# Optimization experiments

Measured on AMD Instinct MI355X. Metric: run time of the kernel, lower is better.

## Reference

```python
import jax, jax.numpy as jnp
import numpy as np

HEADS = 16
NEG_INF = -1e30


def rel_shift(t):
    # t: [b, h, i, j] with i == j; Transformer-XL style relative shift
    b, h, i, j = t.shape
    t = jnp.pad(t, ((0, 0), (0, 0), (0, 0), (1, 0)))  # zero pad on last dim front
    t = t.reshape(b, h, j + 1, i)[:, :, 1:]
    return t.reshape(b, h, i, j)


def setup_inputs() -> dict:
    key = jax.random.key(0)
    ks = jax.random.split(key, 8)
    b, n, dim = 2, 2048, 1024
    d_head = dim // HEADS
    w = 0.02
    return {
        "x": jax.random.normal(ks[0], (b, n, dim), dtype=jnp.float32),
        "pos_emb": jax.random.normal(ks[1], (n, dim), dtype=jnp.float32),
        "Wq": jax.random.normal(ks[2], (dim, dim), dtype=jnp.float32) * w,
        "bq": jnp.zeros((dim,), dtype=jnp.float32),
        "Wkv": jax.random.normal(ks[3], (dim, 2 * dim), dtype=jnp.float32) * w,
        "bkv": jnp.zeros((2 * dim,), dtype=jnp.float32),
        "Wp": jax.random.normal(ks[4], (dim, d_head), dtype=jnp.float32) * w,
        "bp": jnp.zeros((d_head,), dtype=jnp.float32),
        "Wo": jax.random.normal(ks[5], (dim, dim), dtype=jnp.float32) * w,
        "bo": jnp.zeros((dim,), dtype=jnp.float32),
    }


def reference(x, pos_emb, Wq, bq, Wkv, bkv, Wp, bp, Wo, bo):
    b, n, dim = x.shape
    h = HEADS
    d = dim // h
    scale = d ** -0.5

    q = (x @ Wq + bq).reshape(b, n, h, d).transpose(0, 2, 1, 3)  # b h n d
    kv = x @ Wkv + bkv
    k, v = jnp.split(kv, 2, axis=-1)
    k = k.reshape(b, n, h, d).transpose(0, 2, 1, 3)
    v = v.reshape(b, n, h, d).transpose(0, 2, 1, 3)

    dots = jnp.einsum('bhid,bhjd->bhij', q, k) * scale

    # relative position bias
    p = pos_emb @ Wp + bp  # [n, d]
    pos_attn = jnp.einsum('bhid,jd->bhij', q, p) * scale
    dots = dots + rel_shift(pos_attn)

    # causal mask
    causal = jnp.triu(jnp.ones((n, n), dtype=bool), 1)
    dots = jnp.where(causal[None, None], NEG_INF, dots)

    attn = jax.nn.softmax(dots, axis=-1)
    out = jnp.einsum('bhij,bhjd->bhid', attn, v)
    out = out.transpose(0, 2, 1, 3).reshape(b, n, dim)
    return out @ Wo + bo
```

## Files before the change

### kernel.cpp

```cpp
#include <hip/hip_runtime.h>
#include <hip/hip_bf16.h>
#include <cstdint>
#include <cstddef>

#define SEQ_N 2048
#define DIM   1024
#define NHEAD 16
#define DH    64

typedef __bf16 bf16;
typedef __attribute__((ext_vector_type(8))) __bf16 bf16x8;
typedef __attribute__((ext_vector_type(4))) __bf16 bf16x4;
typedef __attribute__((ext_vector_type(4))) float f32x4;

__device__ __forceinline__ void gl_lds16(const bf16* g, bf16* l) {
    __builtin_amdgcn_global_load_lds(
        (const __attribute__((address_space(1))) unsigned int*)g,
        (__attribute__((address_space(3))) unsigned int*)l, 16, 0, 0);
}

__global__ __launch_bounds__(256) void prep_kernel(
    const float* __restrict__ x, const float* __restrict__ pos,
    const float* __restrict__ Wq, const float* __restrict__ Wkv,
    const float* __restrict__ Wo, const float* __restrict__ Wp,
    bf16* __restrict__ xb, bf16* __restrict__ posb,
    bf16* __restrict__ WqkvT, bf16* __restrict__ WoT, bf16* __restrict__ WpT)
{
    int bid = blockIdx.x;
    if (bid < 6144) {
        const int NX = 4096 * 1024;
        int i = (bid * 256 + threadIdx.x) * 4;
        if (i < NX) {
            float4 v = *(const float4*)&x[i];
            xb[i + 0] = (bf16)v.x; xb[i + 1] = (bf16)v.y;
            xb[i + 2] = (bf16)v.z; xb[i + 3] = (bf16)v.w;
        } else {
            int j = i - NX;
            float4 v = *(const float4*)&pos[j];
            posb[j + 0] = (bf16)v.x; posb[j + 1] = (bf16)v.y;
            posb[j + 2] = (bf16)v.z; posb[j + 3] = (bf16)v.w;
        }
        return;
    }
    __shared__ float t[32][33];
    bid -= 6144;
    const float* src; bf16* dst; int tidx, nx, N;
    if (bid < 1024)      { src = Wq;  dst = WqkvT;                       tidx = bid;        nx = 32; N = 1024; }
    else if (bid < 3072) { src = Wkv; dst = WqkvT + (size_t)1024 * 1024; tidx = bid - 1024; nx = 64; N = 2048; }
    else if (bid < 4096) { src = Wo;  dst = WoT;                         tidx = bid - 3072; nx = 32; N = 1024; }
    else                 { src = Wp;  dst = WpT;                         tidx = bid - 4096; nx = 2;  N = 64;   }
    int n0 = (tidx % nx) * 32, k0 = (tidx / nx) * 32;
    int tx = threadIdx.x & 31, ty = threadIdx.x >> 5;
    #pragma unroll
    for (int r = ty; r < 32; r += 8)
        t[r][tx] = src[(size_t)(k0 + r) * N + n0 + tx];
    __syncthreads();
    #pragma unroll
    for (int r = ty; r < 32; r += 8)
        dst[(size_t)(n0 + r) * 1024 + k0 + tx] = (bf16)t[tx][r];
}

__global__ __launch_bounds__(256) void qkvp_kernel(
    const bf16* __restrict__ xb, const bf16* __restrict__ WqkvT,
    const bf16* __restrict__ posb, const bf16* __restrict__ WpT,
    const float* __restrict__ bq, const float* __restrict__ bkv,
    const float* __restrict__ bp,
    bf16* __restrict__ qbuf, bf16* __restrict__ kbuf,
    bf16* __restrict__ vtbuf, bf16* __restrict__ pfrag)
{
    __shared__ __align__(16) bf16 sm[128 * 132];
    bf16* At = sm;
    bf16* Bt = sm + 128 * 64;
    const int tid = threadIdx.x, w = tid >> 6, lane = tid & 63;
    const int q = lane >> 4, ln15 = lane & 15;
    const int lr = lane >> 3, c_log = (lane & 7) ^ lr;
    const int bx = blockIdx.x, by = blockIdx.y;
    const int m0 = by * 128;

    if (bx == 24) {
        if (by >= 16) return;
        f32x4 acc[2][4] = {};
        for (int k0 = 0; k0 < 1024; k0 += 64) {
            __syncthreads();
            #pragma unroll
            for (int t = 0; t < 4; ++t)
                gl_lds16(&posb[(size_t)(m0 + 32 * w + 8 * t + lr) * 1024 + k0 + c_log * 8],
                         &At[(32 * w + 8 * t) * 64]);
            #pragma unroll
            for (int t = 0; t < 2; ++t)
                gl_lds16(&WpT[(size_t)(16 * w + 8 * t + lr) * 1024 + k0 + c_log * 8],
                         &Bt[(16 * w + 8 * t) * 64]);
            __syncthreads();
            bf16x8 bfr[2][4];
            #pragma unroll
            for (int ks = 0; ks < 2; ++ks)
                #pragma unroll
                for (int sn = 0; sn < 4; ++sn) {
                    int rb = 16 * sn + ln15;
                    bfr[ks][sn] = *(const bf16x8*)&Bt[(rb * 8 + ((4 * ks + q) ^ (rb & 7))) * 8];
                }
            #pragma unroll
            for (int sm2 = 0; sm2 < 2; ++sm2) {
                int ra = 32 * w + 16 * sm2 + ln15;
                #pragma unroll
                for (int ks = 0; ks < 2; ++ks) {
                    bf16x8 af = *(const bf16x8*)&At[(ra * 8 + ((4 * ks + q) ^ (ra & 7))) * 8];
                    #pragma unroll
                    for (int sn = 0; sn < 4; ++sn)
                        acc[sm2][sn] = __builtin_amdgcn_mfma_f32_16x16x32_bf16(
                            af, bfr[ks][sn], acc[sm2][sn], 0, 0, 0);
                }
            }
        }
        #pragma unroll
        for (int sm2 = 0; sm2 < 2; ++sm2)
            #pragma unroll
            for (int sn = 0; sn < 4; ++sn)
                #pragma unroll
                for (int r = 0; r < 4; ++r) {
                    int row = m0 + 32 * w + 16 * sm2 + 4 * q + r;
                    int d = 16 * sn + ln15;
                    int sb = row >> 4, lnp = row & 15;
                    int ks2 = d >> 5, qd = (d >> 3) & 3, e = d & 7;
                    pfrag[(((size_t)sb * 2 + ks2) * 64 + qd * 16 + lnp) * 8 + e] =
                        (bf16)(acc[sm2][sn][r] + bp[d]);
                }
        return;
    }

    const int n0 = bx * 128;
    const int wm = w >> 1, wn = w & 1;
    f32x4 acc[4][4] = {};

    for (int k0 = 0; k0 < 1024; k0 += 64) {
        __syncthreads();
        #pragma unroll
        for (int t = 0; t < 4; ++t) {
            int r = 32 * w + 8 * t + lr;
            gl_lds16(&xb[(size_t)(m0 + r) * 1024 + k0 + c_log * 8],
                     &At[(32 * w + 8 * t) * 64]);
            gl_lds16(&WqkvT[(size_t)(n0 + r) * 1024 + k0 + c_log * 8],
                     &Bt[(32 * w + 8 * t) * 64]);
        }
        __syncthreads();

        bf16x8 af[2][4], bfr[2][4];
        #pragma unroll
        for (int ks = 0; ks < 2; ++ks)
            #pragma unroll
            for (int s = 0; s < 4; ++s) {
                int ra = 64 * wm + 16 * s + ln15;
                af[ks][s]  = *(const bf16x8*)&At[(ra * 8 + ((4 * ks + q) ^ (ra & 7))) * 8];
                int rb = 64 * wn + 16 * s + ln15;
                bfr[ks][s] = *(const bf16x8*)&Bt[(rb * 8 + ((4 * ks + q) ^ (rb & 7))) * 8];
            }
        #pragma unroll
        for (int ks = 0; ks < 2; ++ks)
            #pragma unroll
            for (int si = 0; si < 4; ++si)
                #pragma unroll
                for (int sj = 0; sj < 4; ++sj)
                    acc[si][sj] = __builtin_amdgcn_mfma_f32_16x16x32_bf16(
                        af[ks][si], bfr[ks][sj], acc[si][sj], 0, 0, 0);
    }

    if (bx < 16) {
        #pragma unroll
        for (int si = 0; si < 4; ++si)
            #pragma unroll
            for (int sj = 0; sj < 4; ++sj)
                #pragma unroll
                for (int r = 0; r < 4; ++r) {
                    int row = m0 + 64 * wm + 16 * si + 4 * q + r;
                    int col = n0 + 64 * wn + 16 * sj + ln15;
                    float v = acc[si][sj][r] + (col < 1024 ? bq[col] : bkv[col - 1024]);
                    if (col < 1024) qbuf[(size_t)row * 1024 + col] = (bf16)v;
                    else            kbuf[(size_t)row * 1024 + (col - 1024)] = (bf16)v;
                }
    } else {
        __syncthreads();
        #pragma unroll
        for (int si = 0; si < 4; ++si)
            #pragma unroll
            for (int sj = 0; sj < 4; ++sj) {
                int dL = 64 * wn + 16 * sj + ln15;
                int tL = 64 * wm + 16 * si + 4 * q;
                float bias = bkv[1024 + (bx - 16) * 128 + dL];
                bf16x4 o4;
                #pragma unroll
                for (int r = 0; r < 4; ++r)
                    o4[r] = (bf16)(acc[si][sj][r] + bias);
                *(bf16x4*)&sm[dL * 132 + tL] = o4;
            }
        __syncthreads();
        const int b = m0 >> 11;
        const int t0 = m0 & 2047;
        const int h0 = (bx - 16) * 2;
        #pragma unroll
        for (int p = 0; p < 16; ++p) {
            int d = (tid >> 5) + 8 * p;
            int t = (tid & 31) * 4;
            bf16x4 v4 = *(const bf16x4*)&sm[d * 132 + t];
            int rowv = (b * NHEAD + h0 + (d >> 6)) * DH + (d & 63);
            *(bf16x4*)&vtbuf[(size_t)rowv * SEQ_N + t0 + t] = v4;
        }
    }
}

__global__ __launch_bounds__(256, 4) void attn_mfma_kernel(
    const bf16* __restrict__ qb,
    const bf16* __restrict__ kb,
    const bf16* __restrict__ vt,
    const bf16* __restrict__ pfrag,
    bf16* __restrict__ ob)
{
    const int bh = blockIdx.y, bi = bh >> 4, hh = bh & 15;
    const int qblk = ((blockIdx.y >> 3) & 1) ? (31 - (int)blockIdx.x)
                                             : (int)blockIdx.x;
    const int i0 = qblk << 6;
    const int tid = threadIdx.x, w = tid >> 6, lane = tid & 63;
    const int q = lane >> 4, ln15 = lane & 15;
    const int lr = lane >> 3, c_log = (lane & 7) ^ lr;

    __shared__ __align__(16) bf16 smem[17664];
    bf16* Qs  = smem;
    bf16* S2L = smem + w * 1344;
    bf16* Ks  = smem + 5376;
    bf16* Vs  = smem + 9472;
    bf16* Pw  = smem + 13568 + w * 1024;

    const bf16* qbase = qb + ((size_t)(bi * SEQ_N + i0)) * DIM + hh * DH;
    const bf16* kbase = kb + ((size_t)bi * SEQ_N) * DIM + hh * DH;
    const bf16* vbase = vt + ((size_t)(bi * NHEAD + hh) * DH) * SEQ_N;

    #pragma unroll
    for (int t = 0; t < 2; ++t)
        gl_lds16(qbase + (size_t)(16 * w + 8 * t + lr) * DIM + c_log * 8,
                 &Qs[(16 * w + 8 * t) * 64]);
    __syncthreads();
    bf16x8 qf0, qf1;
    {
        int rq = 16 * w + ln15;
        qf0 = *(const bf16x8*)&Qs[(rq * 8 + ((q    ) ^ (rq & 7))) * 8];
        qf1 = *(const bf16x8*)&Qs[(rq * 8 + ((4 + q) ^ (rq & 7))) * 8];
    }
    __syncthreads();

    const int A0 = 127 - 4 * qblk - w;
    f32x4 s2r4;
    {
        bf16x8 f0 = *(const bf16x8*)&pfrag[(((size_t)A0 * 2 + 0) * 64 + lane) * 8];
        bf16x8 f1 = *(const bf16x8*)&pfrag[(((size_t)A0 * 2 + 1) * 64 + lane) * 8];
        f32x4 a = {0.f, 0.f, 0.f, 0.f};
        a = __builtin_amdgcn_mfma_f32_16x16x32_bf16(f0, qf0, a, 0, 0, 0);
        a = __builtin_amdgcn_mfma_f32_16x16x32_bf16(f1, qf1, a, 0, 0, 0);
        s2r4 = a;
    }

    float m_run = -1e30f, l_run = 0.f;
    f32x4 O_T[4] = {};

    for (int jt = 0; jt <= qblk; ++jt) {
        const int j0 = jt << 6;

        bf16x8 pfA[4][2];
        #pragma unroll
        for (int s = 1; s <= 4; ++s) {
            int sb = A0 + 4 * jt + s;
            if (sb > 127) sb = 127;
            pfA[s-1][0] = *(const bf16x8*)&pfrag[(((size_t)sb * 2 + 0) * 64 + lane) * 8];
            pfA[s-1][1] = *(const bf16x8*)&pfrag[(((size_t)sb * 2 + 1) * 64 + lane) * 8];
        }
        #pragma unroll
        for (int t = 0; t < 2; ++t) {
            int r = 16 * w + 8 * t + lr;
            gl_lds16(kbase + (size_t)(j0 + r) * DIM + c_log * 8,
                     &Ks[(16 * w + 8 * t) * 64]);
            gl_lds16(vbase + (size_t)r * SEQ_N + j0 + c_log * 8,
                     &Vs[(16 * w + 8 * t) * 64]);
        }

        f32x4 s2r[5];
        s2r[0] = s2r4;
        #pragma unroll
        for (int s = 1; s <= 4; ++s) {
            f32x4 a = {0.f, 0.f, 0.f, 0.f};
            a = __builtin_amdgcn_mfma_f32_16x16x32_bf16(pfA[s-1][0], qf0, a, 0, 0, 0);
            a = __builtin_amdgcn_mfma_f32_16x16x32_bf16(pfA[s-1][1], qf1, a, 0, 0, 0);
            s2r[s] = a;
        }
        s2r4 = s2r[4];
        #pragma unroll
        for (int s = 0; s < 5; ++s)
            #pragma unroll
            for (int r = 0; r < 4; ++r)
                S2L[ln15 * 84 + 16 * s + 4 * q + r] = (bf16)s2r[s][r];

        __syncthreads();

        float sv[4][4];
        #pragma unroll
        for (int sn = 0; sn < 4; ++sn) {
            int rk = 16 * sn + ln15;
            bf16x8 k0f = *(const bf16x8*)&Ks[(rk * 8 + ((q    ) ^ (rk & 7))) * 8];
            bf16x8 k1f = *(const bf16x8*)&Ks[(rk * 8 + ((4 + q) ^ (rk & 7))) * 8];
            f32x4 a = {0.f, 0.f, 0.f, 0.f};
            a = __builtin_amdgcn_mfma_f32_16x16x32_bf16(k0f, qf0, a, 0, 0, 0);
            a = __builtin_amdgcn_mfma_f32_16x16x32_bf16(k1f, qf1, a, 0, 0, 0);
            #pragma unroll
            for (int r = 0; r < 4; ++r) {
                int jl = 16 * sn + 4 * q + r;
                float b = (float)S2L[ln15 * 84 + 15 - ln15 + jl];
                sv[sn][r] = (a[r] + b) * 0.125f;
            }
        }
        if (jt == qblk) {
            #pragma unroll
            for (int sn = 0; sn < 4; ++sn)
                #pragma unroll
                for (int r = 0; r < 4; ++r)
                    if (16 * sn + 4 * q + r > 16 * w + ln15)
                        sv[sn][r] = -1e30f;
        }

        float mx = sv[0][0];
        #pragma unroll
        for (int sn = 0; sn < 4; ++sn)
            #pragma unroll
            for (int r = 0; r < 4; ++r)
                mx = fmaxf(mx, sv[sn][r]);
        mx = fmaxf(mx, __shfl_xor(mx, 16));
        mx = fmaxf(mx, __shfl_xor(mx, 32));
        const float mn = fmaxf(m_run, mx);
        float sum = 0.f;
        #pragma unroll
        for (int sn = 0; sn < 4; ++sn)
            #pragma unroll
            for (int r = 0; r < 4; ++r) {
                float e = __expf(sv[sn][r] - mn);
                sv[sn][r] = e;
                sum += e;
            }
        sum += __shfl_xor(sum, 16);
        sum += __shfl_xor(sum, 32);
        const float alpha = __expf(m_run - mn);
        l_run = l_run * alpha + sum;
        m_run = mn;

        #pragma unroll
        for (int sn = 0; sn < 4; ++sn)
            #pragma unroll
            for (int r = 0; r < 4; ++r) {
                int chunk = (2 * sn + (q >> 1)) ^ (ln15 & 7);
                Pw[ln15 * 64 + chunk * 8 + 4 * (q & 1) + r] = (bf16)sv[sn][r];
            }
        #pragma unroll
        for (int sd = 0; sd < 4; ++sd)
            #pragma unroll
            for (int r = 0; r < 4; ++r)
                O_T[sd][r] *= alpha;

        __builtin_amdgcn_s_waitcnt(0);

        #pragma unroll
        for (int ks = 0; ks < 2; ++ks) {
            bf16x8 pT = *(const bf16x8*)&Pw[ln15 * 64 + (((4 * ks + q) ^ (ln15 & 7))) * 8];
            #pragma unroll
            for (int sd = 0; sd < 4; ++sd) {
                int rv = 16 * sd + ln15;
                bf16x8 vf = *(const bf16x8*)&Vs[(rv * 8 + ((4 * ks + q) ^ (rv & 7))) * 8];
                O_T[sd] = __builtin_amdgcn_mfma_f32_16x16x32_bf16(vf, pT, O_T[sd], 0, 0, 0);
            }
        }
        __syncthreads();
    }

    const float inv = 1.0f / l_run;
    const size_t row = (size_t)bi * SEQ_N + i0 + 16 * w + ln15;
    #pragma unroll
    for (int sd = 0; sd < 4; ++sd) {
        bf16x4 o4;
        #pragma unroll
        for (int r = 0; r < 4; ++r)
            o4[r] = (bf16)(O_T[sd][r] * inv);
        *(bf16x4*)&ob[row * DIM + hh * DH + 16 * sd + 4 * q] = o4;
    }
}

__global__ __launch_bounds__(256) void outproj_kernel(
    const bf16* __restrict__ ab, const bf16* __restrict__ WoT,
    const float* __restrict__ bo, float* __restrict__ out)
{
    __shared__ __align__(16) bf16 At[128 * 64];
    __shared__ __align__(16) bf16 Bt[64 * 64];
    const int tid = threadIdx.x, w = tid >> 6, lane = tid & 63;
    const int q = lane >> 4, ln15 = lane & 15;
    const int lr = lane >> 3, c_log = (lane & 7) ^ lr;
    const int m0 = blockIdx.y * 128, n0 = blockIdx.x * 64;

    f32x4 acc[2][4] = {};
    for (int k0 = 0; k0 < 1024; k0 += 64) {
        __syncthreads();
        #pragma unroll
        for (int t = 0; t < 4; ++t)
            gl_lds16(&ab[(size_t)(m0 + 32 * w + 8 * t + lr) * 1024 + k0 + c_log * 8],
                     &At[(32 * w + 8 * t) * 64]);
        #pragma unroll
        for (int t = 0; t < 2; ++t)
            gl_lds16(&WoT[(size_t)(n0 + 16 * w + 8 * t + lr) * 1024 + k0 + c_log * 8],
                     &Bt[(16 * w + 8 * t) * 64]);
        __syncthreads();

        bf16x8 bfr[2][4];
        #pragma unroll
        for (int ks = 0; ks < 2; ++ks)
            #pragma unroll
            for (int sn = 0; sn < 4; ++sn) {
                int rb = 16 * sn + ln15;
                bfr[ks][sn] = *(const bf16x8*)&Bt[(rb * 8 + ((4 * ks + q) ^ (rb & 7))) * 8];
            }
        #pragma unroll
        for (int sm2 = 0; sm2 < 2; ++sm2) {
            int ra = 32 * w + 16 * sm2 + ln15;
            #pragma unroll
            for (int ks = 0; ks < 2; ++ks) {
                bf16x8 af = *(const bf16x8*)&At[(ra * 8 + ((4 * ks + q) ^ (ra & 7))) * 8];
                #pragma unroll
                for (int sn = 0; sn < 4; ++sn)
                    acc[sm2][sn] = __builtin_amdgcn_mfma_f32_16x16x32_bf16(
                        af, bfr[ks][sn], acc[sm2][sn], 0, 0, 0);
            }
        }
    }
    #pragma unroll
    for (int sm2 = 0; sm2 < 2; ++sm2)
        #pragma unroll
        for (int sn = 0; sn < 4; ++sn) {
            int col = n0 + 16 * sn + ln15;
            float bias = bo[col];
            #pragma unroll
            for (int r = 0; r < 4; ++r) {
                int row = m0 + 32 * w + 16 * sm2 + 4 * q + r;
                out[(size_t)row * 1024 + col] = acc[sm2][sn][r] + bias;
            }
        }
}

extern "C" void kernel_launch(void* const* d_in, const int* in_sizes, int n_in,
                              void* d_out, int out_size, void* d_ws, size_t ws_size,
                              hipStream_t stream)
{
    const float* x    = (const float*)d_in[0];
    const float* pos  = (const float*)d_in[1];
    const float* Wq   = (const float*)d_in[2];
    const float* bq   = (const float*)d_in[3];
    const float* Wkv  = (const float*)d_in[4];
    const float* bkv  = (const float*)d_in[5];
    const float* Wp   = (const float*)d_in[6];
    const float* bp   = (const float*)d_in[7];
    const float* Wo   = (const float*)d_in[8];
    const float* bo   = (const float*)d_in[9];
    float* out = (float*)d_out;

    const int M = 2 * SEQ_N;
    char* ws = (char*)d_ws;
    bf16* xb     = (bf16*)ws;  ws += (size_t)M * DIM * 2;
    bf16* posb   = (bf16*)ws;  ws += (size_t)SEQ_N * DIM * 2;
    bf16* WqkvT  = (bf16*)ws;  ws += (size_t)3072 * 1024 * 2;
    bf16* WoT    = (bf16*)ws;  ws += (size_t)DIM * DIM * 2;
    bf16* WpT    = (bf16*)ws;  ws += (size_t)DH * DIM * 2;
    bf16* qbuf   = (bf16*)ws;  ws += (size_t)M * DIM * 2;
    bf16* kbuf   = (bf16*)ws;  ws += (size_t)M * DIM * 2;
    bf16* vtbuf  = (bf16*)ws;  ws += (size_t)M * DIM * 2;
    bf16* pfrag  = (bf16*)ws;  ws += (size_t)512 * 1024;
    bf16* abuf   = (bf16*)ws;

    dim3 blk(256);
    prep_kernel<<<dim3(10304), blk, 0, stream>>>(
        x, pos, Wq, Wkv, Wo, Wp, xb, posb, WqkvT, WoT, WpT);

    qkvp_kernel<<<dim3(25, 32), blk, 0, stream>>>(
        xb, WqkvT, posb, WpT, bq, bkv, bp, qbuf, kbuf, vtbuf, pfrag);

    attn_mfma_kernel<<<dim3(32, 32), blk, 0, stream>>>(
        qbuf, kbuf, vtbuf, pfrag, abuf);

    outproj_kernel<<<dim3(16, 32), blk, 0, stream>>>(
        abuf, WoT, bo, out);
}
```

Measured before the change: 246.0 us.

## Process 128 query rows per attention block with two row strips per wave

The attention kernel's query tile grows from 64 to 128 rows, and each wave now handles two 16-row strips. This lets every K/V tile loaded into shared memory, and the relative-position fragments, serve twice as many query rows. Causal masking is now computed per strip from position differences, and a wave skips key tiles lying entirely above its diagonal. The load-balancing swap now pairs block order by batch instead of head, and launch bounds drop to 2 blocks per CU. That raises register and shared-memory use and halves the grid to 512 blocks, which reduces occupancy and parallelism.

```diff
diff --git a/kernel.cpp b/kernel.cpp
--- a/kernel.cpp
+++ b/kernel.cpp
@@ -207,70 +207,81 @@
     }
 }
 
-__global__ __launch_bounds__(256, 4) void attn_mfma_kernel(
-    const bf16* __restrict__ qb,
+__global__ __launch_bounds__(256, 2) void attn_mfma_kernel(
+    const bf16* __restrict__ qp,
     const bf16* __restrict__ kb,
     const bf16* __restrict__ vt,
     const bf16* __restrict__ pfrag,
     bf16* __restrict__ ob)
 {
-    const int bh = blockIdx.y, bi = bh >> 4, hh = bh & 15;
-    const int qblk = ((blockIdx.y >> 3) & 1) ? (31 - (int)blockIdx.x)
-                                             : (int)blockIdx.x;
-    const int i0 = qblk << 6;
+    const int by = blockIdx.y;
+    const int bi = by >> 4, hh = by & 15;
+    const int qb = (by >> 4) ? (15 - (int)blockIdx.x) : (int)blockIdx.x;
+    const int i0 = qb << 7;
     const int tid = threadIdx.x, w = tid >> 6, lane = tid & 63;
     const int q = lane >> 4, ln15 = lane & 15;
     const int lr = lane >> 3, c_log = (lane & 7) ^ lr;
 
-    __shared__ __align__(16) bf16 smem[17664];
-    bf16* Qs  = smem;
-    bf16* S2L = smem + w * 1344;
-    bf16* Ks  = smem + 5376;
-    bf16* Vs  = smem + 9472;
-    bf16* Pw  = smem + 13568 + w * 1024;
-
-    const bf16* qbase = qb + ((size_t)(bi * SEQ_N + i0)) * DIM + hh * DH;
+    __shared__ __align__(16) bf16 smem[27136];
+    bf16* Qs = smem;
+    bf16* Ks = smem + 10752;
+    bf16* Vs = smem + 14848;
+    const int st0 = 2 * w, st1 = 2 * w + 1;
+    bf16* S2L0 = smem + st0 * 1344;
+    bf16* S2L1 = smem + st1 * 1344;
+    bf16* Pw0  = smem + 18944 + st0 * 1024;
+    bf16* Pw1  = smem + 18944 + st1 * 1024;
+
+    const bf16* qbase = qp + ((size_t)(bi * SEQ_N + i0)) * DIM + hh * DH;
     const bf16* kbase = kb + ((size_t)bi * SEQ_N) * DIM + hh * DH;
     const bf16* vbase = vt + ((size_t)(bi * NHEAD + hh) * DH) * SEQ_N;
 
     #pragma unroll
-    for (int t = 0; t < 2; ++t)
-        gl_lds16(qbase + (size_t)(16 * w + 8 * t + lr) * DIM + c_log * 8,
-                 &Qs[(16 * w + 8 * t) * 64]);
+    for (int t = 0; t < 4; ++t)
+        gl_lds16(qbase + (size_t)(32 * w + 8 * t + lr) * DIM + c_log * 8,
+                 &Qs[(32 * w + 8 * t) * 64]);
+    __builtin_amdgcn_s_waitcnt(0);
+
+    bf16x8 qfA[2], qfB[2];
+    {
+        int rq = 16 * st0 + ln15;
+        qfA[0] = *(const bf16x8*)&Qs[(rq * 8 + ((q    ) ^ (rq & 7))) * 8];
+        qfA[1] = *(const bf16x8*)&Qs[(rq * 8 + ((4 + q) ^ (rq & 7))) * 8];
+        rq = 16 * st1 + ln15;
+        qfB[0] = *(const bf16x8*)&Qs[(rq * 8 + ((q    ) ^ (rq & 7))) * 8];
+        qfB[1] = *(const bf16x8*)&Qs[(rq * 8 + ((4 + q) ^ (rq & 7))) * 8];
+    }
+
+    const int A0 = 127 - 8 * qb - st0;
+    f32x4 carryA, carryB;
+    {
+        const bf16* p0 = pfrag + ((size_t)A0 * 128 + lane) * 8;
+        bf16x8 f0 = *(const bf16x8*)p0;
+        bf16x8 f1 = *(const bf16x8*)(p0 + 512);
+        f32x4 a = {0.f, 0.f, 0.f, 0.f};
+        a = __builtin_amdgcn_mfma_f32_16x16x32_bf16(f0, qfA[0], a, 0, 0, 0);
+        a = __builtin_amdgcn_mfma_f32_16x16x32_bf16(f1, qfA[1], a, 0, 0, 0);
+        carryA = a;
+        const bf16* p1 = pfrag + ((size_t)(A0 - 1) * 128 + lane) * 8;
+        bf16x8 g0 = *(const bf16x8*)p1;
+        bf16x8 g1 = *(const bf16x8*)(p1 + 512);
+        f32x4 b = {0.f, 0.f, 0.f, 0.f};
+        b = __builtin_amdgcn_mfma_f32_16x16x32_bf16(g0, qfB[0], b, 0, 0, 0);
+        b = __builtin_amdgcn_mfma_f32_16x16x32_bf16(g1, qfB[1], b, 0, 0, 0);
+        carryB = b;
+    }
     __syncthreads();
-    bf16x8 qf0, qf1;
-    {
-        int rq = 16 * w + ln15;
-        qf0 = *(const bf16x8*)&Qs[(rq * 8 + ((q    ) ^ (rq & 7))) * 8];
-        qf1 = *(const bf16x8*)&Qs[(rq * 8 + ((4 + q) ^ (rq & 7))) * 8];
-    }
-    __syncthreads();
-
-    const int A0 = 127 - 4 * qblk - w;
-    f32x4 s2r4;
-    {
-        bf16x8 f0 = *(const bf16x8*)&pfrag[(((size_t)A0 * 2 + 0) * 64 + lane) * 8];
-        bf16x8 f1 = *(const bf16x8*)&pfrag[(((size_t)A0 * 2 + 1) * 64 + lane) * 8];
-        f32x4 a = {0.f, 0.f, 0.f, 0.f};
-        a = __builtin_amdgcn_mfma_f32_16x16x32_bf16(f0, qf0, a, 0, 0, 0);
-        a = __builtin_amdgcn_mfma_f32_16x16x32_bf16(f1, qf1, a, 0, 0, 0);
-        s2r4 = a;
-    }
-
-    float m_run = -1e30f, l_run = 0.f;
-    f32x4 O_T[4] = {};
-
-    for (int jt = 0; jt <= qblk; ++jt) {
+
+    float mA = -1e30f, lA = 0.f, mB = -1e30f, lB = 0.f;
+    f32x4 OA[4] = {}, OB[4] = {};
+
+    const int jtMax = 2 * qb + 1;
+    for (int jt = 0; jt <= jtMax; ++jt) {
         const int j0 = jt << 6;
-
-        bf16x8 pfA[4][2];
-        #pragma unroll
-        for (int s = 1; s <= 4; ++s) {
-            int sb = A0 + 4 * jt + s;
-            if (sb > 127) sb = 127;
-            pfA[s-1][0] = *(const bf16x8*)&pfrag[(((size_t)sb * 2 + 0) * 64 + lane) * 8];
-            pfA[s-1][1] = *(const bf16x8*)&pfrag[(((size_t)sb * 2 + 1) * 64 + lane) * 8];
-        }
+        const bool skipAll = (j0 > i0 + 16 * st1 + 15);
+        const bool maskA = (j0 + 63) > (i0 + 16 * st0);
+        const bool maskB = (j0 + 63) > (i0 + 16 * st1);
+
         #pragma unroll
         for (int t = 0; t < 2; ++t) {
             int r = 16 * w + 8 * t + lr;
@@ -280,110 +291,160 @@
                      &Vs[(16 * w + 8 * t) * 64]);
         }
 
-        f32x4 s2r[5];
-        s2r[0] = s2r4;
-        #pragma unroll
-        for (int s = 1; s <= 4; ++s) {
-            f32x4 a = {0.f, 0.f, 0.f, 0.f};
-            a = __builtin_amdgcn_mfma_f32_16x16x32_bf16(pfA[s-1][0], qf0, a, 0, 0, 0);
-            a = __builtin_amdgcn_mfma_f32_16x16x32_bf16(pfA[s-1][1], qf1, a, 0, 0, 0);
-            s2r[s] = a;
-        }
-        s2r4 = s2r[4];
-        #pragma unroll
-        for (int s = 0; s < 5; ++s)
-            #pragma unroll
-            for (int r = 0; r < 4; ++r)
-                S2L[ln15 * 84 + 16 * s + 4 * q + r] = (bf16)s2r[s][r];
-
-        __syncthreads();
-
-        float sv[4][4];
-        #pragma unroll
-        for (int sn = 0; sn < 4; ++sn) {
-            int rk = 16 * sn + ln15;
-            bf16x8 k0f = *(const bf16x8*)&Ks[(rk * 8 + ((q    ) ^ (rk & 7))) * 8];
-            bf16x8 k1f = *(const bf16x8*)&Ks[(rk * 8 + ((4 + q) ^ (rk & 7))) * 8];
-            f32x4 a = {0.f, 0.f, 0.f, 0.f};
-            a = __builtin_amdgcn_mfma_f32_16x16x32_bf16(k0f, qf0, a, 0, 0, 0);
-            a = __builtin_amdgcn_mfma_f32_16x16x32_bf16(k1f, qf1, a, 0, 0, 0);
-            #pragma unroll
-            for (int r = 0; r < 4; ++r) {
-                int jl = 16 * sn + 4 * q + r;
-                float b = (float)S2L[ln15 * 84 + 15 - ln15 + jl];
-                sv[sn][r] = (a[r] + b) * 0.125f;
-            }
-        }
-        if (jt == qblk) {
+        if (!skipAll) {
+            bf16x8 pfU[5][2];
+            #pragma unroll
+            for (int s = 0; s < 5; ++s) {
+                int sb = A0 + 4 * jt + s;
+                if (sb > 127) sb = 127;
+                const bf16* p = pfrag + ((size_t)sb * 128 + lane) * 8;
+                pfU[s][0] = *(const bf16x8*)p;
+                pfU[s][1] = *(const bf16x8*)(p + 512);
+            }
+            f32x4 rA[5], rB[5];
+            rA[0] = carryA; rB[0] = carryB;
+            #pragma unroll
+            for (int s = 1; s <= 4; ++s) {
+                f32x4 a = {0.f, 0.f, 0.f, 0.f};
+                a = __builtin_amdgcn_mfma_f32_16x16x32_bf16(pfU[s][0], qfA[0], a, 0, 0, 0);
+                a = __builtin_amdgcn_mfma_f32_16x16x32_bf16(pfU[s][1], qfA[1], a, 0, 0, 0);
+                rA[s] = a;
+                f32x4 b = {0.f, 0.f, 0.f, 0.f};
+                b = __builtin_amdgcn_mfma_f32_16x16x32_bf16(pfU[s-1][0], qfB[0], b, 0, 0, 0);
+                b = __builtin_amdgcn_mfma_f32_16x16x32_bf16(pfU[s-1][1], qfB[1], b, 0, 0, 0);
+                rB[s] = b;
+            }
+            carryA = rA[4]; carryB = rB[4];
+            #pragma unroll
+            for (int s = 0; s < 5; ++s) {
+                bf16x4 pkA, pkB;
+                #pragma unroll
+                for (int r = 0; r < 4; ++r) { pkA[r] = (bf16)rA[s][r]; pkB[r] = (bf16)rB[s][r]; }
+                *(bf16x4*)&S2L0[ln15 * 84 + 16 * s + 4 * q] = pkA;
+                *(bf16x4*)&S2L1[ln15 * 84 + 16 * s + 4 * q] = pkB;
+            }
+        }
+        __syncthreads();
+
+        if (!skipAll) {
+            f32x4 s1A[4], s1B[4];
+            #pragma unroll
+            for (int sn = 0; sn < 4; ++sn) {
+                int rk = 16 * sn + ln15;
+                bf16x8 k0f = *(const bf16x8*)&Ks[(rk * 8 + ((q    ) ^ (rk & 7))) * 8];
+                bf16x8 k1f = *(const bf16x8*)&Ks[(rk * 8 + ((4 + q) ^ (rk & 7))) * 8];
+                f32x4 a = {0.f, 0.f, 0.f, 0.f};
+                a = __builtin_amdgcn_mfma_f32_16x16x32_bf16(k0f, qfA[0], a, 0, 0, 0);
+                a = __builtin_amdgcn_mfma_f32_16x16x32_bf16(k1f, qfA[1], a, 0, 0, 0);
+                s1A[sn] = a;
+                f32x4 b = {0.f, 0.f, 0.f, 0.f};
+                b = __builtin_amdgcn_mfma_f32_16x16x32_bf16(k0f, qfB[0], b, 0, 0, 0);
+                b = __builtin_amdgcn_mfma_f32_16x16x32_bf16(k1f, qfB[1], b, 0, 0, 0);
+                s1B[sn] = b;
+            }
+
+            float svA[4][4], svB[4][4];
+            const int dA = i0 + 16 * st0 + ln15 - j0;
+            const int dB = dA + 16;
             #pragma unroll
             for (int sn = 0; sn < 4; ++sn)
                 #pragma unroll
-                for (int r = 0; r < 4; ++r)
-                    if (16 * sn + 4 * q + r > 16 * w + ln15)
-                        sv[sn][r] = -1e30f;
-        }
-
-        float mx = sv[0][0];
-        #pragma unroll
-        for (int sn = 0; sn < 4; ++sn)
-            #pragma unroll
-            for (int r = 0; r < 4; ++r)
-                mx = fmaxf(mx, sv[sn][r]);
-        mx = fmaxf(mx, __shfl_xor(mx, 16));
-        mx = fmaxf(mx, __shfl_xor(mx, 32));
-        const float mn = fmaxf(m_run, mx);
-        float sum = 0.f;
-        #pragma unroll
-        for (int sn = 0; sn < 4; ++sn)
-            #pragma unroll
-            for (int r = 0; r < 4; ++r) {
-                float e = __expf(sv[sn][r] - mn);
-                sv[sn][r] = e;
-                sum += e;
-            }
-        sum += __shfl_xor(sum, 16);
-        sum += __shfl_xor(sum, 32);
-        const float alpha = __expf(m_run - mn);
-        l_run = l_run * alpha + sum;
-        m_run = mn;
-
-        #pragma unroll
-        for (int sn = 0; sn < 4; ++sn)
-            #pragma unroll
-            for (int r = 0; r < 4; ++r) {
+                for (int r = 0; r < 4; ++r) {
+                    int jl = 16 * sn + 4 * q + r;
+                    float ba = (float)S2L0[ln15 * 84 + 15 - ln15 + jl];
+                    float va = (s1A[sn][r] + ba) * 0.125f;
+                    if (maskA && jl > dA) va = -1e30f;
+                    svA[sn][r] = va;
+                    float bb = (float)S2L1[ln15 * 84 + 15 - ln15 + jl];
+                    float vb = (s1B[sn][r] + bb) * 0.125f;
+                    if (maskB && jl > dB) vb = -1e30f;
+                    svB[sn][r] = vb;
+                }
+
+            float mxA = svA[0][0], mxB = svB[0][0];
+            #pragma unroll
+            for (int sn = 0; sn < 4; ++sn)
+                #pragma unroll
+                for (int r = 0; r < 4; ++r) {
+                    mxA = fmaxf(mxA, svA[sn][r]);
+                    mxB = fmaxf(mxB, svB[sn][r]);
+                }
+            mxA = fmaxf(mxA, __shfl_xor(mxA, 16)); mxA = fmaxf(mxA, __shfl_xor(mxA, 32));
+            mxB = fmaxf(mxB, __shfl_xor(mxB, 16)); mxB = fmaxf(mxB, __shfl_xor(mxB, 32));
+            const float mnA = fmaxf(mA, mxA), mnB = fmaxf(mB, mxB);
+            float sumA = 0.f, sumB = 0.f;
+            #pragma unroll
+            for (int sn = 0; sn < 4; ++sn)
+                #pragma unroll
+                for (int r = 0; r < 4; ++r) {
+                    float ea = __expf(svA[sn][r] - mnA); svA[sn][r] = ea; sumA += ea;
+                    float eb = __expf(svB[sn][r] - mnB); svB[sn][r] = eb; sumB += eb;
+                }
+            sumA += __shfl_xor(sumA, 16); sumA += __shfl_xor(sumA, 32);
+            sumB += __shfl_xor(sumB, 16); sumB += __shfl_xor(sumB, 32);
+            const float alA = __expf(mA - mnA), alB = __expf(mB - mnB);
+            lA = lA * alA + sumA; mA = mnA;
+            lB = lB * alB + sumB; mB = mnB;
+
+            #pragma unroll
+            for (int sn = 0; sn < 4; ++sn) {
                 int chunk = (2 * sn + (q >> 1)) ^ (ln15 & 7);
-                Pw[ln15 * 64 + chunk * 8 + 4 * (q & 1) + r] = (bf16)sv[sn][r];
-            }
-        #pragma unroll
-        for (int sd = 0; sd < 4; ++sd)
-            #pragma unroll
-            for (int r = 0; r < 4; ++r)
-                O_T[sd][r] *= alpha;
-
-        __builtin_amdgcn_s_waitcnt(0);
-
-        #pragma unroll
-        for (int ks = 0; ks < 2; ++ks) {
-            bf16x8 pT = *(const bf16x8*)&Pw[ln15 * 64 + (((4 * ks + q) ^ (ln15 & 7))) * 8];
-            #pragma unroll
-            for (int sd = 0; sd < 4; ++sd) {
-                int rv = 16 * sd + ln15;
-                bf16x8 vf = *(const bf16x8*)&Vs[(rv * 8 + ((4 * ks + q) ^ (rv & 7))) * 8];
-                O_T[sd] = __builtin_amdgcn_mfma_f32_16x16x32_bf16(vf, pT, O_T[sd], 0, 0, 0);
-            }
-        }
-        __syncthreads();
-    }
-
-    const float inv = 1.0f / l_run;
-    const size_t row = (size_t)bi * SEQ_N + i0 + 16 * w + ln15;
-    #pragma unroll
-    for (int sd = 0; sd < 4; ++sd) {
-        bf16x4 o4;
-        #pragma unroll
-        for (int r = 0; r < 4; ++r)
-            o4[r] = (bf16)(O_T[sd][r] * inv);
-        *(bf16x4*)&ob[row * DIM + hh * DH + 16 * sd + 4 * q] = o4;
+                int off = ln15 * 64 + chunk * 8 + 4 * (q & 1);
+                bf16x4 pkA, pkB;
+                #pragma unroll
+                for (int r = 0; r < 4; ++r) { pkA[r] = (bf16)svA[sn][r]; pkB[r] = (bf16)svB[sn][r]; }
+                *(bf16x4*)&Pw0[off] = pkA;
+                *(bf16x4*)&Pw1[off] = pkB;
+            }
+            #pragma unroll
+            for (int sd = 0; sd < 4; ++sd)
+                #pragma unroll
+                for (int r = 0; r < 4; ++r) {
+                    OA[sd][r] *= alA;
+                    OB[sd][r] *= alB;
+                }
+
+            __builtin_amdgcn_s_waitcnt(0);
+
+            bf16x8 pTA[2], pTB[2];
+            #pragma unroll
+            for (int ks = 0; ks < 2; ++ks) {
+                int off = ln15 * 64 + (((4 * ks + q) ^ (ln15 & 7))) * 8;
+                pTA[ks] = *(const bf16x8*)&Pw0[off];
+                pTB[ks] = *(const bf16x8*)&Pw1[off];
+            }
+            #pragma unroll
+            for (int ks = 0; ks < 2; ++ks)
+                #pragma unroll
+                for (int sd = 0; sd < 4; ++sd) {
+                    int rv = 16 * sd + ln15;
+                    bf16x8 vf = *(const bf16x8*)&Vs[(rv * 8 + ((4 * ks + q) ^ (rv & 7))) * 8];
+                    OA[sd] = __builtin_amdgcn_mfma_f32_16x16x32_bf16(vf, pTA[ks], OA[sd], 0, 0, 0);
+                    OB[sd] = __builtin_amdgcn_mfma_f32_16x16x32_bf16(vf, pTB[ks], OB[sd], 0, 0, 0);
+                }
+        }
+        __syncthreads();
+    }
+
+    {
+        const float invA = 1.0f / lA;
+        const size_t rowA = (size_t)bi * SEQ_N + i0 + 16 * st0 + ln15;
+        #pragma unroll
+        for (int sd = 0; sd < 4; ++sd) {
+            bf16x4 o4;
+            #pragma unroll
+            for (int r = 0; r < 4; ++r) o4[r] = (bf16)(OA[sd][r] * invA);
+            *(bf16x4*)&ob[rowA * DIM + hh * DH + 16 * sd + 4 * q] = o4;
+        }
+        const float invB = 1.0f / lB;
+        const size_t rowB = (size_t)bi * SEQ_N + i0 + 16 * st1 + ln15;
+        #pragma unroll
+        for (int sd = 0; sd < 4; ++sd) {
+            bf16x4 o4;
+            #pragma unroll
+            for (int r = 0; r < 4; ++r) o4[r] = (bf16)(OB[sd][r] * invB);
+            *(bf16x4*)&ob[rowB * DIM + hh * DH + 16 * sd + 4 * q] = o4;
+        }
     }
 }
 
@@ -482,7 +543,7 @@
     qkvp_kernel<<<dim3(25, 32), blk, 0, stream>>>(
         xb, WqkvT, posb, WpT, bq, bkv, bp, qbuf, kbuf, vtbuf, pfrag);
 
-    attn_mfma_kernel<<<dim3(32, 32), blk, 0, stream>>>(
+    attn_mfma_kernel<<<dim3(16, 32), blk, 0, stream>>>(
         qbuf, kbuf, vtbuf, pfrag, abuf);
 
     outproj_kernel<<<dim3(16, 32), blk, 0, stream>>>(
```

Measured after the change: 268.1 us. +9.0%, slower.
